# Optimization experiments

Measured on AMD Instinct MI355X. Metric: run time of the kernel, lower is better.

Reference implementation:

```python
import jax, jax.numpy as jnp
import numpy as np

B, N, D = 4, 4096, 256

def setup_inputs() -> dict:
    key = jax.random.key(0)
    k1, = jax.random.split(key, 1)
    x = jax.random.normal(k1, (B, N, D), dtype=jnp.float32)
    attn_mask = jnp.ones((B, 1, N), dtype=jnp.int32)
    pad_mask = jnp.ones((B, 1, N), dtype=jnp.int32)
    return {"x": x, "attn_mask": attn_mask, "pad_mask": pad_mask, "dim_": D}

def reference(x, attn_mask, pad_mask, dim_):
    # adj is None -> scores = x @ x^T / sqrt(d)
    scale = jnp.sqrt(jnp.asarray(x.shape[-1], x.dtype))
    scores = jnp.einsum('bnd,bmd->bnm', x, x) / scale  # [B, N, N]
    # NOTE: original calls non-in-place masked_fill and discards the result,
    # so pad_mask / attn_mask have no effect on the output (faithful).
    prob = jax.nn.softmax(scores, axis=-1)
    # dropout is identity in inference mode
    return jnp.einsum('bnm,bmd->bnd', prob, x)
```

## Files before the change

kernel.cpp:

```cpp
#include <hip/hip_runtime.h>

typedef __attribute__((ext_vector_type(8))) short short8;
typedef __attribute__((ext_vector_type(4))) float f32x4;
typedef __attribute__((ext_vector_type(4))) unsigned int u32x4;

#define NTOK 4096
#define DIM  256
#define P_STRIDE 72
#define TILE_ELEMS 32768

__device__ __forceinline__ unsigned pack2bf(float a, float b) {
  unsigned ua = __builtin_bit_cast(unsigned, a) + 0x8000u;
  unsigned ub = __builtin_bit_cast(unsigned, b) + 0x8000u;
  return __builtin_amdgcn_perm(ub, ua, 0x07060302u);
}

__global__ __launch_bounds__(256, 4)
void prep_kernel(const float* __restrict__ X, unsigned short* __restrict__ Img) {
  __shared__ __align__(16) unsigned short rowbf[8 * 256];
  const int b    = blockIdx.x & 3;
  const int sub  = blockIdx.x >> 2;
  const int t    = sub >> 3;
  const int part = sub & 7;
  const int tid  = threadIdx.x;
  const float* src = X + ((size_t)b * NTOK + t * 64 + part * 8) * DIM;
  unsigned short* dst = Img + ((size_t)(b * 64 + t)) * TILE_ELEMS;
  {
    const int r = tid >> 5;
    const int c = tid & 31;
    const float* s = src + r * DIM + c * 8;
    f32x4 f0 = *(const f32x4*)s;
    f32x4 f1 = *(const f32x4*)(s + 4);
    union { unsigned u[4]; u32x4 v; } p;
    p.u[0] = pack2bf(f0[0], f0[1]);
    p.u[1] = pack2bf(f0[2], f0[3]);
    p.u[2] = pack2bf(f1[0], f1[1]);
    p.u[3] = pack2bf(f1[2], f1[3]);
    const int gr = part * 8 + r;
    *(u32x4*)(dst + gr * 256 + ((c ^ (gr & 7)) << 3)) = p.v;
    *(u32x4*)(&rowbf[r * 256 + c * 8]) = p.v;
  }
  __syncthreads();
  {
    const int d = tid;
    union { unsigned short s[8]; u32x4 v; } p;
    #pragma unroll
    for (int i = 0; i < 8; ++i) p.s[i] = rowbf[i * 256 + d];
    *(u32x4*)(dst + 16384 + part * 2048 + d * 8) = p.v;
  }
}

__device__ __forceinline__ void pv_step(const unsigned short* __restrict__ pr,
                                        const unsigned short* __restrict__ kt,
                                        f32x4 (&o)[2][4],
                                        int qh, int role, int quad, int ln) {
  #pragma unroll
  for (int ks = 0; ks < 2; ++ks) {
    const int pos = (ks * 4 + quad) ^ ((ln >> 3) << 1);
    short8 ap[2], bv[4];
    #pragma unroll
    for (int s = 0; s < 2; ++s) {
      const int r = qh * 32 + s * 16 + ln;
      ap[s] = *(const short8*)(&pr[r * P_STRIDE + (pos << 3)]);
    }
    const unsigned short* kb = kt + (ks * 4 + quad) * 2048 + (role * 64 + ln) * 8;
    #pragma unroll
    for (int dt = 0; dt < 4; ++dt) bv[dt] = *(const short8*)(kb + dt * 128);
    #pragma unroll
    for (int s = 0; s < 2; ++s)
      #pragma unroll
      for (int dt = 0; dt < 4; ++dt)
        o[s][dt] = __builtin_amdgcn_mfma_f32_16x16x32_bf16(ap[s], bv[dt], o[s][dt], 0, 0, 0);
  }
}

__global__ __launch_bounds__(512, 1)
void fa_kernel(const unsigned short* __restrict__ Img, float* __restrict__ Out) {
  __shared__ __align__(16) unsigned short ksb[2][16384];
  __shared__ __align__(16) unsigned short ktb[2][16384];
  __shared__ __align__(16) unsigned short pb[2][64 * P_STRIDE];
  __shared__ float lbuf[64][4];

  const int tid  = threadIdx.x;
  const int b    = blockIdx.x & 3;
  const int qblk = blockIdx.x >> 2;
  const int wave = tid >> 6;
  const int lane = tid & 63;
  const int ln   = lane & 15;
  const int quad = lane >> 4;
  const int swz  = ln & 7;
  const int qh   = wave & 1;
  const int role = wave >> 1;

  const unsigned short* imgb  = Img + (size_t)b * 64 * TILE_ELEMS;
  const char*           imgbc = (const char*)imgb;

  short8 aQ[2][8];
  #pragma unroll
  for (int s = 0; s < 2; ++s) {
    const unsigned short* qrow =
        imgb + (size_t)qblk * TILE_ELEMS + (qh * 32 + s * 16 + ln) * 256;
    #pragma unroll
    for (int ds = 0; ds < 8; ++ds)
      aQ[s][ds] = *(const short8*)(qrow + (((ds * 4 + quad) ^ swz) << 3));
  }

  f32x4 o[2][4];
  #pragma unroll
  for (int s = 0; s < 2; ++s)
    #pragma unroll
    for (int dt = 0; dt < 4; ++dt) o[s][dt] = (f32x4)(0.0f);
  float lrow[2][4] = {{0.f,0.f,0.f,0.f},{0.f,0.f,0.f,0.f}};

  const float c2 = 0.0901684400f;

  const int pwPos = ((role * 2 + (ln >> 3)) ^ ((quad >> 1) << 1)) << 3;
  const int pwCol = ln & 7;

  const bool dmaKs = wave < 4;
  const int  dmaQ  = wave & 3;
  const char* gK = imgbc + (size_t)dmaQ * 8192 + (size_t)lane * 16;

  if (dmaKs) {
    #pragma unroll
    for (int i = 0; i < 8; ++i)
      __builtin_amdgcn_global_load_lds(
          (const __attribute__((address_space(1))) unsigned*)(gK + i * 1024),
          (__attribute__((address_space(3))) unsigned*)(&ksb[0][dmaQ * 4096 + i * 512]),
          16, 0, 0);
  }

  for (int t = 0; t < 64; ++t) {
    __syncthreads();
    const int buf = t & 1;

    if (dmaKs) {
      if (t < 63) {
        const char* g = gK + (size_t)(t + 1) * 65536;
        unsigned short* l = &ksb[buf ^ 1][dmaQ * 4096];
        #pragma unroll
        for (int i = 0; i < 8; ++i)
          __builtin_amdgcn_global_load_lds(
              (const __attribute__((address_space(1))) unsigned*)(g + i * 1024),
              (__attribute__((address_space(3))) unsigned*)(l + i * 512),
              16, 0, 0);
      }
    } else {
      const char* g = gK + (size_t)t * 65536 + 32768;
      unsigned short* l = &ktb[buf][dmaQ * 4096];
      #pragma unroll
      for (int i = 0; i < 8; ++i)
        __builtin_amdgcn_global_load_lds(
            (const __attribute__((address_space(1))) unsigned*)(g + i * 1024),
            (__attribute__((address_space(3))) unsigned*)(l + i * 512),
            16, 0, 0);
    }

    f32x4 sf0 = (f32x4)(0.0f), sf1 = (f32x4)(0.0f);
    {
      const unsigned short* krow = &ksb[buf][(role * 16 + ln) * 256];
      #pragma unroll
      for (int ds = 0; ds < 8; ++ds) {
        short8 bk = *(const short8*)(krow + (((ds * 4 + quad) ^ swz) << 3));
        sf0 = __builtin_amdgcn_mfma_f32_16x16x32_bf16(aQ[0][ds], bk, sf0, 0, 0, 0);
        sf1 = __builtin_amdgcn_mfma_f32_16x16x32_bf16(aQ[1][ds], bk, sf1, 0, 0, 0);
      }
    }
    {
      unsigned short* pw = pb[buf];
      #pragma unroll
      for (int j = 0; j < 4; ++j) {
        float p0 = __builtin_amdgcn_exp2f(sf0[j] * c2);
        float p1 = __builtin_amdgcn_exp2f(sf1[j] * c2);
        lrow[0][j] += p0;
        lrow[1][j] += p1;
        unsigned q0 = __builtin_bit_cast(unsigned, p0);
        unsigned q1 = __builtin_bit_cast(unsigned, p1);
        unsigned n0 = (unsigned)__builtin_amdgcn_mov_dpp((int)q0, 0xB1, 0xF, 0xF, true);
        unsigned n1 = (unsigned)__builtin_amdgcn_mov_dpp((int)q1, 0xB1, 0xF, 0xF, true);
        if ((ln & 1) == 0) {
          const int r0 = qh * 32 + quad * 4 + j;
          unsigned d0 = pack2bf(__builtin_bit_cast(float, q0), __builtin_bit_cast(float, n0));
          unsigned d1 = pack2bf(__builtin_bit_cast(float, q1), __builtin_bit_cast(float, n1));
          *(unsigned*)(&pw[r0 * P_STRIDE + pwPos + pwCol]) = d0;
          *(unsigned*)(&pw[(r0 + 16) * P_STRIDE + pwPos + pwCol]) = d1;
        }
      }
    }

    if (t > 0)
      pv_step(pb[buf ^ 1], ktb[buf ^ 1], o, qh, role, quad, ln);
  }

  __syncthreads();
  pv_step(pb[1], ktb[1], o, qh, role, quad, ln);

  #pragma unroll
  for (int off = 1; off < 16; off <<= 1)
    #pragma unroll
    for (int s = 0; s < 2; ++s)
      #pragma unroll
      for (int j = 0; j < 4; ++j)
        lrow[s][j] += __shfl_xor(lrow[s][j], off, 64);
  if (ln == 0) {
    #pragma unroll
    for (int s = 0; s < 2; ++s)
      #pragma unroll
      for (int j = 0; j < 4; ++j)
        lbuf[qh * 32 + s * 16 + quad * 4 + j][role] = lrow[s][j];
  }
  __syncthreads();

  #pragma unroll
  for (int s = 0; s < 2; ++s) {
    float* outp = Out + (size_t)(b * NTOK + qblk * 64 + qh * 32 + s * 16) * DIM + role * 64;
    #pragma unroll
    for (int j = 0; j < 4; ++j) {
      const int row = s * 16 + quad * 4 + j;
      f32x4 lv = *(const f32x4*)lbuf[qh * 32 + row];
      const float rl = 1.0f / (lv[0] + lv[1] + lv[2] + lv[3]);
      #pragma unroll
      for (int dt = 0; dt < 4; ++dt)
        outp[(size_t)(quad * 4 + j) * DIM + dt * 16 + ln] = o[s][dt][j] * rl;
    }
  }
}

extern "C" void kernel_launch(void* const* d_in, const int* in_sizes, int n_in,
                              void* d_out, int out_size, void* d_ws, size_t ws_size,
                              hipStream_t stream) {
  const float* X = (const float*)d_in[0];
  float* Out = (float*)d_out;
  unsigned short* Img = (unsigned short*)d_ws;
  (void)in_sizes; (void)n_in; (void)out_size; (void)ws_size;
  hipLaunchKernelGGL(prep_kernel, dim3(2048), dim3(256), 0, stream, X, Img);
  hipLaunchKernelGGL(fa_kernel, dim3(256), dim3(512), 0, stream, Img, Out);
}
```

Baseline: 172.7 us.

## Switch attention kernel to 32x32x16 MFMA with two key tiles per step and register V

Replaces the 16x16x32 MFMA tiling with 32x32x16 MFMA tiles for both QK^T and PV. Each iteration now processes two 64-key tiles, halving the loop count. V fragments are loaded straight from global memory into registers instead of being staged in LDS. The P buffer layout and swizzle are redone for the new fragment shapes, and the row-sum buffer reuses P's shared memory. The aims are higher MFMA efficiency, fewer barriers and less LDS traffic, at the cost of more register pressure and exposed global-load latency for V.

Result: no change. 174.1 us (+0.8%).

```diff
diff --git a/kernel.cpp b/kernel.cpp
--- a/kernel.cpp
+++ b/kernel.cpp
@@ -2,11 +2,11 @@
 
 typedef __attribute__((ext_vector_type(8))) short short8;
 typedef __attribute__((ext_vector_type(4))) float f32x4;
+typedef __attribute__((ext_vector_type(16))) float f32x16;
 typedef __attribute__((ext_vector_type(4))) unsigned int u32x4;
 
 #define NTOK 4096
 #define DIM  256
-#define P_STRIDE 72
 #define TILE_ELEMS 32768
 
 __device__ __forceinline__ unsigned pack2bf(float a, float b) {
@@ -50,104 +50,68 @@
   }
 }
 
-__device__ __forceinline__ void pv_step(const unsigned short* __restrict__ pr,
-                                        const unsigned short* __restrict__ kt,
-                                        f32x4 (&o)[2][4],
-                                        int qh, int role, int quad, int ln) {
-  #pragma unroll
-  for (int ks = 0; ks < 2; ++ks) {
-    const int pos = (ks * 4 + quad) ^ ((ln >> 3) << 1);
-    short8 ap[2], bv[4];
-    #pragma unroll
-    for (int s = 0; s < 2; ++s) {
-      const int r = qh * 32 + s * 16 + ln;
-      ap[s] = *(const short8*)(&pr[r * P_STRIDE + (pos << 3)]);
-    }
-    const unsigned short* kb = kt + (ks * 4 + quad) * 2048 + (role * 64 + ln) * 8;
-    #pragma unroll
-    for (int dt = 0; dt < 4; ++dt) bv[dt] = *(const short8*)(kb + dt * 128);
-    #pragma unroll
-    for (int s = 0; s < 2; ++s)
-      #pragma unroll
-      for (int dt = 0; dt < 4; ++dt)
-        o[s][dt] = __builtin_amdgcn_mfma_f32_16x16x32_bf16(ap[s], bv[dt], o[s][dt], 0, 0, 0);
-  }
-}
-
-__global__ __launch_bounds__(512, 1)
+__global__ __launch_bounds__(512, 2)
 void fa_kernel(const unsigned short* __restrict__ Img, float* __restrict__ Out) {
-  __shared__ __align__(16) unsigned short ksb[2][16384];
-  __shared__ __align__(16) unsigned short ktb[2][16384];
-  __shared__ __align__(16) unsigned short pb[2][64 * P_STRIDE];
-  __shared__ float lbuf[64][4];
+  __shared__ __align__(16) unsigned short ksb[2][32768];
+  __shared__ __align__(16) unsigned short pb[2][8192];
 
   const int tid  = threadIdx.x;
   const int b    = blockIdx.x & 3;
   const int qblk = blockIdx.x >> 2;
   const int wave = tid >> 6;
   const int lane = tid & 63;
-  const int ln   = lane & 15;
-  const int quad = lane >> 4;
-  const int swz  = ln & 7;
+  const int l5   = lane & 31;
+  const int h    = lane >> 5;
+  const int swz  = l5 & 7;
   const int qh   = wave & 1;
-  const int role = wave >> 1;
+  const int kg   = wave >> 1;
 
   const unsigned short* imgb  = Img + (size_t)b * 64 * TILE_ELEMS;
   const char*           imgbc = (const char*)imgb;
 
-  short8 aQ[2][8];
+  short8 aQ[16];
+  {
+    const unsigned short* qrow =
+        imgb + (size_t)qblk * TILE_ELEMS + (qh * 32 + l5) * 256;
+    #pragma unroll
+    for (int k = 0; k < 16; ++k)
+      aQ[k] = *(const short8*)(qrow + (((k * 2 + h) ^ swz) << 3));
+  }
+
+  f32x16 o0 = (f32x16)(0.0f), o1 = (f32x16)(0.0f);
+  float lsum[16];
   #pragma unroll
-  for (int s = 0; s < 2; ++s) {
-    const unsigned short* qrow =
-        imgb + (size_t)qblk * TILE_ELEMS + (qh * 32 + s * 16 + ln) * 256;
-    #pragma unroll
-    for (int ds = 0; ds < 8; ++ds)
-      aQ[s][ds] = *(const short8*)(qrow + (((ds * 4 + quad) ^ swz) << 3));
-  }
-
-  f32x4 o[2][4];
-  #pragma unroll
-  for (int s = 0; s < 2; ++s)
-    #pragma unroll
-    for (int dt = 0; dt < 4; ++dt) o[s][dt] = (f32x4)(0.0f);
-  float lrow[2][4] = {{0.f,0.f,0.f,0.f},{0.f,0.f,0.f,0.f}};
+  for (int r = 0; r < 16; ++r) lsum[r] = 0.f;
 
   const float c2 = 0.0901684400f;
 
-  const int pwPos = ((role * 2 + (ln >> 3)) ^ ((quad >> 1) << 1)) << 3;
-  const int pwCol = ln & 7;
-
-  const bool dmaKs = wave < 4;
-  const int  dmaQ  = wave & 3;
-  const char* gK = imgbc + (size_t)dmaQ * 8192 + (size_t)lane * 16;
-
-  if (dmaKs) {
+  const int psBase = (qh * 32 + ((l5 & 1) << 4) + 4 * h) * 128 + (l5 & 6);
+  const int cXb    = (kg * 4 + (l5 >> 3)) ^ (h << 2);
+
+  const char* vbase = imgbc + 32768 + h * 4096 + (size_t)(kg * 64 + l5) * 16;
+
+  const int dp = wave >> 2, dq = wave & 3;
+  const char* gKs = imgbc + (size_t)dp * 65536 + dq * 8192 + (size_t)lane * 16;
+  {
+    unsigned short* l = &ksb[0][dp * 16384 + dq * 4096];
     #pragma unroll
     for (int i = 0; i < 8; ++i)
       __builtin_amdgcn_global_load_lds(
-          (const __attribute__((address_space(1))) unsigned*)(gK + i * 1024),
-          (__attribute__((address_space(3))) unsigned*)(&ksb[0][dmaQ * 4096 + i * 512]),
+          (const __attribute__((address_space(1))) unsigned*)(gKs + i * 1024),
+          (__attribute__((address_space(3))) unsigned*)(l + i * 512),
           16, 0, 0);
   }
 
-  for (int t = 0; t < 64; ++t) {
+  short8 vF[2][8];
+
+  #pragma unroll 1
+  for (int t = 0; t < 32; ++t) {
     __syncthreads();
     const int buf = t & 1;
 
-    if (dmaKs) {
-      if (t < 63) {
-        const char* g = gK + (size_t)(t + 1) * 65536;
-        unsigned short* l = &ksb[buf ^ 1][dmaQ * 4096];
-        #pragma unroll
-        for (int i = 0; i < 8; ++i)
-          __builtin_amdgcn_global_load_lds(
-              (const __attribute__((address_space(1))) unsigned*)(g + i * 1024),
-              (__attribute__((address_space(3))) unsigned*)(l + i * 512),
-              16, 0, 0);
-      }
-    } else {
-      const char* g = gK + (size_t)t * 65536 + 32768;
-      unsigned short* l = &ktb[buf][dmaQ * 4096];
+    if (t < 31) {
+      const char* g = gKs + (size_t)(2 * (t + 1)) * 65536;
+      unsigned short* l = &ksb[buf ^ 1][dp * 16384 + dq * 4096];
       #pragma unroll
       for (int i = 0; i < 8; ++i)
         __builtin_amdgcn_global_load_lds(
@@ -156,73 +120,102 @@
             16, 0, 0);
     }
 
-    f32x4 sf0 = (f32x4)(0.0f), sf1 = (f32x4)(0.0f);
+    f32x16 sfA = (f32x16)(0.0f), sfB = (f32x16)(0.0f);
     {
-      const unsigned short* krow = &ksb[buf][(role * 16 + ln) * 256];
-      #pragma unroll
-      for (int ds = 0; ds < 8; ++ds) {
-        short8 bk = *(const short8*)(krow + (((ds * 4 + quad) ^ swz) << 3));
-        sf0 = __builtin_amdgcn_mfma_f32_16x16x32_bf16(aQ[0][ds], bk, sf0, 0, 0, 0);
-        sf1 = __builtin_amdgcn_mfma_f32_16x16x32_bf16(aQ[1][ds], bk, sf1, 0, 0, 0);
-      }
-    }
+      const unsigned short* krow =
+          &ksb[buf][(kg >> 1) * 16384 + ((kg & 1) * 32 + l5) * 256];
+      #pragma unroll
+      for (int k = 0; k < 16; k += 2) {
+        short8 b0 = *(const short8*)(krow + (((k * 2 + h) ^ swz) << 3));
+        short8 b1 = *(const short8*)(krow + (((k * 2 + 2 + h) ^ swz) << 3));
+        sfA = __builtin_amdgcn_mfma_f32_32x32x16_bf16(aQ[k], b0, sfA, 0, 0, 0);
+        sfB = __builtin_amdgcn_mfma_f32_32x32x16_bf16(aQ[k + 1], b1, sfB, 0, 0, 0);
+      }
+    }
+    f32x16 sf = sfA + sfB;
+
+    float p[16];
+    #pragma unroll
+    for (int r = 0; r < 16; ++r) {
+      p[r] = __builtin_amdgcn_exp2f(sf[r] * c2);
+      lsum[r] += p[r];
+    }
+    unsigned pd[8];
+    #pragma unroll
+    for (int j = 0; j < 8; ++j) {
+      unsigned pj  = __builtin_bit_cast(unsigned, p[j]);
+      unsigned pj8 = __builtin_bit_cast(unsigned, p[j + 8]);
+      unsigned dj  = (unsigned)__builtin_amdgcn_mov_dpp((int)pj, 0xB1, 0xF, 0xF, true);
+      unsigned dj8 = (unsigned)__builtin_amdgcn_mov_dpp((int)pj8, 0xB1, 0xF, 0xF, true);
+      float lo = (l5 & 1) ? __builtin_bit_cast(float, dj8) : p[j];
+      float hi = (l5 & 1) ? p[j + 8] : __builtin_bit_cast(float, dj);
+      pd[j] = pack2bf(lo, hi);
+    }
+
+    if (t > 0) {
+      const unsigned short* prow = pb[buf ^ 1] + (qh * 32 + l5) * 128;
+      #pragma unroll
+      for (int ks = 0; ks < 8; ++ks) {
+        short8 pA = *(const short8*)(prow + (((ks * 2 + h) ^ swz) << 3));
+        o0 = __builtin_amdgcn_mfma_f32_32x32x16_bf16(pA, vF[0][ks], o0, 0, 0, 0);
+        o1 = __builtin_amdgcn_mfma_f32_32x32x16_bf16(pA, vF[1][ks], o1, 0, 0, 0);
+      }
+    }
+
+    {
+      const char* vb = vbase + (size_t)(2 * t) * 65536;
+      #pragma unroll
+      for (int ks = 0; ks < 8; ++ks) {
+        const int off = ks * 8192 + (ks >= 4 ? 32768 : 0);
+        vF[0][ks] = *(const short8*)(vb + off);
+        vF[1][ks] = *(const short8*)(vb + off + 512);
+      }
+    }
+
     {
       unsigned short* pw = pb[buf];
       #pragma unroll
-      for (int j = 0; j < 4; ++j) {
-        float p0 = __builtin_amdgcn_exp2f(sf0[j] * c2);
-        float p1 = __builtin_amdgcn_exp2f(sf1[j] * c2);
-        lrow[0][j] += p0;
-        lrow[1][j] += p1;
-        unsigned q0 = __builtin_bit_cast(unsigned, p0);
-        unsigned q1 = __builtin_bit_cast(unsigned, p1);
-        unsigned n0 = (unsigned)__builtin_amdgcn_mov_dpp((int)q0, 0xB1, 0xF, 0xF, true);
-        unsigned n1 = (unsigned)__builtin_amdgcn_mov_dpp((int)q1, 0xB1, 0xF, 0xF, true);
-        if ((ln & 1) == 0) {
-          const int r0 = qh * 32 + quad * 4 + j;
-          unsigned d0 = pack2bf(__builtin_bit_cast(float, q0), __builtin_bit_cast(float, n0));
-          unsigned d1 = pack2bf(__builtin_bit_cast(float, q1), __builtin_bit_cast(float, n1));
-          *(unsigned*)(&pw[r0 * P_STRIDE + pwPos + pwCol]) = d0;
-          *(unsigned*)(&pw[(r0 + 16) * P_STRIDE + pwPos + pwCol]) = d1;
-        }
-      }
-    }
-
-    if (t > 0)
-      pv_step(pb[buf ^ 1], ktb[buf ^ 1], o, qh, role, quad, ln);
+      for (int j = 0; j < 8; ++j) {
+        const int off = psBase + ((j & 3) + 8 * (j >> 2)) * 128 +
+                        ((cXb ^ (j & 3)) << 3);
+        *(unsigned*)(&pw[off]) = pd[j];
+      }
+    }
   }
 
   __syncthreads();
-  pv_step(pb[1], ktb[1], o, qh, role, quad, ln);
+  {
+    const unsigned short* prow = pb[1] + (qh * 32 + l5) * 128;
+    #pragma unroll
+    for (int ks = 0; ks < 8; ++ks) {
+      short8 pA = *(const short8*)(prow + (((ks * 2 + h) ^ swz) << 3));
+      o0 = __builtin_amdgcn_mfma_f32_32x32x16_bf16(pA, vF[0][ks], o0, 0, 0, 0);
+      o1 = __builtin_amdgcn_mfma_f32_32x32x16_bf16(pA, vF[1][ks], o1, 0, 0, 0);
+    }
+  }
 
   #pragma unroll
-  for (int off = 1; off < 16; off <<= 1)
-    #pragma unroll
-    for (int s = 0; s < 2; ++s)
-      #pragma unroll
-      for (int j = 0; j < 4; ++j)
-        lrow[s][j] += __shfl_xor(lrow[s][j], off, 64);
-  if (ln == 0) {
-    #pragma unroll
-    for (int s = 0; s < 2; ++s)
-      #pragma unroll
-      for (int j = 0; j < 4; ++j)
-        lbuf[qh * 32 + s * 16 + quad * 4 + j][role] = lrow[s][j];
+  for (int off = 1; off < 32; off <<= 1)
+    #pragma unroll
+    for (int r = 0; r < 16; ++r)
+      lsum[r] += __shfl_xor(lsum[r], off, 64);
+
+  float (*lbufF)[4] = (float(*)[4])(&pb[0][0]);
+  if (l5 == 0) {
+    #pragma unroll
+    for (int r = 0; r < 16; ++r)
+      lbufF[qh * 32 + (r & 3) + 8 * (r >> 2) + 4 * h][kg] = lsum[r];
   }
   __syncthreads();
 
+  float* outp = Out + (size_t)(b * NTOK + qblk * 64) * DIM;
   #pragma unroll
-  for (int s = 0; s < 2; ++s) {
-    float* outp = Out + (size_t)(b * NTOK + qblk * 64 + qh * 32 + s * 16) * DIM + role * 64;
-    #pragma unroll
-    for (int j = 0; j < 4; ++j) {
-      const int row = s * 16 + quad * 4 + j;
-      f32x4 lv = *(const f32x4*)lbuf[qh * 32 + row];
-      const float rl = 1.0f / (lv[0] + lv[1] + lv[2] + lv[3]);
-      #pragma unroll
-      for (int dt = 0; dt < 4; ++dt)
-        outp[(size_t)(quad * 4 + j) * DIM + dt * 16 + ln] = o[s][dt][j] * rl;
-    }
+  for (int r = 0; r < 16; ++r) {
+    const int row = qh * 32 + (r & 3) + 8 * (r >> 2) + 4 * h;
+    f32x4 lv = *(const f32x4*)lbufF[row];
+    const float rl = 1.0f / (lv[0] + lv[1] + lv[2] + lv[3]);
+    outp[(size_t)row * DIM + kg * 64 + l5]      = o0[r] * rl;
+    outp[(size_t)row * DIM + kg * 64 + 32 + l5] = o1[r] * rl;
   }
 }
 
```
